# Kernel optimization log

Measured on AMD Instinct MI355X. Metric: run time of the kernel, lower is better.

## Reference

```python
import jax, jax.numpy as jnp
import numpy as np

K = 16  # number of piecewise-linear intervals (fixed in params_set)


def setup_inputs() -> dict:
    key = jax.random.key(0)
    k1, k2 = jax.random.split(key)
    B, S, D = 4, 4096, 2048
    x = jax.random.normal(k1, (B, S, D), dtype=jnp.float32)
    threshold = jnp.ones((1,), dtype=jnp.float32)          # alpha > 0
    theta = 0.1 * jax.random.normal(k2, (K,), dtype=jnp.float32)
    dst = jnp.arange(K, dtype=jnp.float32) / K             # delta * arange(K), delta = 1/K
    return {
        "x": x,
        "threshold": threshold,
        "theta": theta,
        "dst": dst,
        "Qn": 0,
        "Qp": 15,                 # 2**4 - 1 (activation, num_bits=4)
        "num_elements": B * S * D,
    }


def reference(x, threshold, theta, dst, Qn, Qp, num_elements):
    # LCQ_quantizer.forward (non 2-bit-weight path) -> LCQ_fast_core.forward
    s = float(Qp)
    theta_tmp = jax.nn.softmax(theta)                       # softmax over dim 0
    gamma = theta_tmp * K                                   # theta_tmp / delta
    beta = jnp.concatenate(
        [jnp.zeros((1,), theta_tmp.dtype), jnp.cumsum(theta_tmp)[: K - 1]]
    )
    alpha = threshold                                       # shape (1,), broadcasts

    flag_middle = (jnp.abs(x) < alpha).astype(x.dtype)
    flag_high = 1.0 - flag_middle
    x_tmp = jnp.abs(x) / alpha

    # compress: searchsorted bin lookup + piecewise affine
    idx = jnp.searchsorted(dst, x_tmp, side="right")        # in [1, K]
    y = gamma[idx - 1] * (x_tmp - dst[idx - 1]) + beta[idx - 1]
    y_q = jnp.round(y * s) / s                              # uniform round-quantize

    # expand: second searchsorted + inverse affine
    idx_q = jnp.searchsorted(beta, y_q, side="right")       # in [1, K]
    z_mid = (y_q - beta[idx_q - 1]) / gamma[idx_q - 1] + dst[idx_q - 1]

    z = jnp.sign(x) * alpha * (z_mid * flag_middle + flag_high)
    return z
```

## Files before the change

### kernel.cpp

```cpp
#include <hip/hip_runtime.h>
#include <math.h>

#define KB 16

typedef float vf4 __attribute__((ext_vector_type(4)));

__device__ __forceinline__ float lcq_core(float xv, float alpha, float rcp_alpha,
                                          const float2* __restrict__ s_gb,
                                          const float* __restrict__ s_zval)
{
    float a   = fabsf(xv);
    float xt  = __fmul_rn(a, rcp_alpha);
    float t16 = __fmul_rn(xt, 16.0f);
    float jf  = fminf(t16, 15.0f);
    int   j   = (int)jf;
    float2 gb = s_gb[j];
    float dj  = __fmul_rn(floorf(jf), 0.0625f);
    float y   = __fadd_rn(__fmul_rn(gb.x, __fsub_rn(xt, dj)), gb.y);
    float t   = rintf(__fmul_rn(y, 15.0f));
    int   m   = (int)fminf(t, 15.0f);
    float v   = (a < alpha) ? s_zval[m] : 1.0f;
    float r   = __fmul_rn(alpha, v);
    return copysignf(r, xv);
}

__global__ __launch_bounds__(256) void lcq_kernel(
    const float* __restrict__ x,
    const float* __restrict__ thr,
    const float* __restrict__ theta,
    float* __restrict__ out,
    long long n)
{
    __shared__ float2 s_gb[KB];
    __shared__ float  s_zval[KB];
    __shared__ float  s_scal[2];

    if (threadIdx.x == 0) {
        float th[KB];
        float mx = theta[0];
        th[0] = mx;
        #pragma unroll
        for (int i = 1; i < KB; ++i) { th[i] = theta[i]; mx = fmaxf(mx, th[i]); }
        float ex[KB];
        float sum = 0.0f;
        #pragma unroll
        for (int i = 0; i < KB; ++i) { ex[i] = expf(__fsub_rn(th[i], mx)); sum = __fadd_rn(sum, ex[i]); }
        float sm[KB];
        #pragma unroll
        for (int i = 0; i < KB; ++i) sm[i] = __fdiv_rn(ex[i], sum);

        float beta[KB], gamma[KB];
        beta[0] = 0.0f;
        float c = sm[0];
        #pragma unroll
        for (int i = 1; i < KB; ++i) { beta[i] = c; c = __fadd_rn(c, sm[i]); }
        #pragma unroll
        for (int i = 0; i < KB; ++i) gamma[i] = __fmul_rn(sm[i], 16.0f);

        #pragma unroll
        for (int i = 0; i < KB; ++i) s_gb[i] = make_float2(gamma[i], beta[i]);

        for (int m = 0; m < KB; ++m) {
            float yq = __fdiv_rn((float)m, 15.0f);
            int iq = 0;
            #pragma unroll
            for (int i = 1; i < KB; ++i) iq += (beta[i] <= yq) ? 1 : 0;
            s_zval[m] = __fadd_rn(__fdiv_rn(__fsub_rn(yq, beta[iq]), gamma[iq]),
                                  (float)iq * 0.0625f);
        }
        float alpha = thr[0];
        s_scal[0] = alpha;
        s_scal[1] = __fdiv_rn(1.0f, alpha);
    }
    __syncthreads();

    const float alpha = s_scal[0];
    const float rcpa  = s_scal[1];

    const long long tid = (long long)blockIdx.x * blockDim.x + threadIdx.x;
    const long long NT  = (long long)gridDim.x * blockDim.x;
    const long long n4  = n >> 2;

    const vf4* __restrict__ x4 = (const vf4*)x;
    vf4* __restrict__ o4 = (vf4*)out;

    long long i = tid;
    for (; i + 3 * NT < n4; i += 4 * NT) {
        vf4 v0 = __builtin_nontemporal_load(&x4[i]);
        vf4 v1 = __builtin_nontemporal_load(&x4[i + NT]);
        vf4 v2 = __builtin_nontemporal_load(&x4[i + 2 * NT]);
        vf4 v3 = __builtin_nontemporal_load(&x4[i + 3 * NT]);
        vf4 r0, r1, r2, r3;
        r0.x = lcq_core(v0.x, alpha, rcpa, s_gb, s_zval);
        r0.y = lcq_core(v0.y, alpha, rcpa, s_gb, s_zval);
        r0.z = lcq_core(v0.z, alpha, rcpa, s_gb, s_zval);
        r0.w = lcq_core(v0.w, alpha, rcpa, s_gb, s_zval);
        r1.x = lcq_core(v1.x, alpha, rcpa, s_gb, s_zval);
        r1.y = lcq_core(v1.y, alpha, rcpa, s_gb, s_zval);
        r1.z = lcq_core(v1.z, alpha, rcpa, s_gb, s_zval);
        r1.w = lcq_core(v1.w, alpha, rcpa, s_gb, s_zval);
        r2.x = lcq_core(v2.x, alpha, rcpa, s_gb, s_zval);
        r2.y = lcq_core(v2.y, alpha, rcpa, s_gb, s_zval);
        r2.z = lcq_core(v2.z, alpha, rcpa, s_gb, s_zval);
        r2.w = lcq_core(v2.w, alpha, rcpa, s_gb, s_zval);
        r3.x = lcq_core(v3.x, alpha, rcpa, s_gb, s_zval);
        r3.y = lcq_core(v3.y, alpha, rcpa, s_gb, s_zval);
        r3.z = lcq_core(v3.z, alpha, rcpa, s_gb, s_zval);
        r3.w = lcq_core(v3.w, alpha, rcpa, s_gb, s_zval);
        __builtin_nontemporal_store(r0, &o4[i]);
        __builtin_nontemporal_store(r1, &o4[i + NT]);
        __builtin_nontemporal_store(r2, &o4[i + 2 * NT]);
        __builtin_nontemporal_store(r3, &o4[i + 3 * NT]);
    }
    for (; i < n4; i += NT) {
        vf4 v = x4[i];
        vf4 r;
        r.x = lcq_core(v.x, alpha, rcpa, s_gb, s_zval);
        r.y = lcq_core(v.y, alpha, rcpa, s_gb, s_zval);
        r.z = lcq_core(v.z, alpha, rcpa, s_gb, s_zval);
        r.w = lcq_core(v.w, alpha, rcpa, s_gb, s_zval);
        o4[i] = r;
    }
    for (long long k = (n4 << 2) + tid; k < n; k += NT) {
        out[k] = lcq_core(x[k], alpha, rcpa, s_gb, s_zval);
    }
}

extern "C" void kernel_launch(void* const* d_in, const int* in_sizes, int n_in,
                              void* d_out, int out_size, void* d_ws, size_t ws_size,
                              hipStream_t stream) {
    const float* x     = (const float*)d_in[0];
    const float* thr   = (const float*)d_in[1];
    const float* theta = (const float*)d_in[2];
    float* out = (float*)d_out;

    long long n = (long long)in_sizes[0];
    dim3 block(256);
    dim3 grid(2048);
    hipLaunchKernelGGL(lcq_kernel, grid, block, 0, stream, x, thr, theta, out, n);
}
```

Measured before the change: 244.3 us.

## Replace grid-stride loop with one-tile-per-block launch sized to input

```diff
diff --git a/kernel.cpp b/kernel.cpp
--- a/kernel.cpp
+++ b/kernel.cpp
@@ -77,19 +77,17 @@
     const float alpha = s_scal[0];
     const float rcpa  = s_scal[1];
 
-    const long long tid = (long long)blockIdx.x * blockDim.x + threadIdx.x;
-    const long long NT  = (long long)gridDim.x * blockDim.x;
-    const long long n4  = n >> 2;
-
+    const long long n4ll = n >> 2;
     const vf4* __restrict__ x4 = (const vf4*)x;
     vf4* __restrict__ o4 = (vf4*)out;
 
-    long long i = tid;
-    for (; i + 3 * NT < n4; i += 4 * NT) {
-        vf4 v0 = __builtin_nontemporal_load(&x4[i]);
-        vf4 v1 = __builtin_nontemporal_load(&x4[i + NT]);
-        vf4 v2 = __builtin_nontemporal_load(&x4[i + 2 * NT]);
-        vf4 v3 = __builtin_nontemporal_load(&x4[i + 3 * NT]);
+    const unsigned base = blockIdx.x * 1024u + threadIdx.x;
+
+    if ((long long)(blockIdx.x + 1) * 1024ll <= n4ll) {
+        vf4 v0 = __builtin_nontemporal_load(&x4[base]);
+        vf4 v1 = __builtin_nontemporal_load(&x4[base + 256u]);
+        vf4 v2 = __builtin_nontemporal_load(&x4[base + 512u]);
+        vf4 v3 = __builtin_nontemporal_load(&x4[base + 768u]);
         vf4 r0, r1, r2, r3;
         r0.x = lcq_core(v0.x, alpha, rcpa, s_gb, s_zval);
         r0.y = lcq_core(v0.y, alpha, rcpa, s_gb, s_zval);
@@ -107,22 +105,29 @@
         r3.y = lcq_core(v3.y, alpha, rcpa, s_gb, s_zval);
         r3.z = lcq_core(v3.z, alpha, rcpa, s_gb, s_zval);
         r3.w = lcq_core(v3.w, alpha, rcpa, s_gb, s_zval);
-        __builtin_nontemporal_store(r0, &o4[i]);
-        __builtin_nontemporal_store(r1, &o4[i + NT]);
-        __builtin_nontemporal_store(r2, &o4[i + 2 * NT]);
-        __builtin_nontemporal_store(r3, &o4[i + 3 * NT]);
-    }
-    for (; i < n4; i += NT) {
-        vf4 v = x4[i];
-        vf4 r;
-        r.x = lcq_core(v.x, alpha, rcpa, s_gb, s_zval);
-        r.y = lcq_core(v.y, alpha, rcpa, s_gb, s_zval);
-        r.z = lcq_core(v.z, alpha, rcpa, s_gb, s_zval);
-        r.w = lcq_core(v.w, alpha, rcpa, s_gb, s_zval);
-        o4[i] = r;
-    }
-    for (long long k = (n4 << 2) + tid; k < n; k += NT) {
-        out[k] = lcq_core(x[k], alpha, rcpa, s_gb, s_zval);
+        __builtin_nontemporal_store(r0, &o4[base]);
+        __builtin_nontemporal_store(r1, &o4[base + 256u]);
+        __builtin_nontemporal_store(r2, &o4[base + 512u]);
+        __builtin_nontemporal_store(r3, &o4[base + 768u]);
+    } else {
+        #pragma unroll
+        for (int k = 0; k < 4; ++k) {
+            long long i = (long long)base + k * 256;
+            if (i < n4ll) {
+                vf4 v = x4[i];
+                vf4 r;
+                r.x = lcq_core(v.x, alpha, rcpa, s_gb, s_zval);
+                r.y = lcq_core(v.y, alpha, rcpa, s_gb, s_zval);
+                r.z = lcq_core(v.z, alpha, rcpa, s_gb, s_zval);
+                r.w = lcq_core(v.w, alpha, rcpa, s_gb, s_zval);
+                o4[i] = r;
+            }
+        }
+        if (blockIdx.x == gridDim.x - 1) {
+            for (long long k = (n4ll << 2) + threadIdx.x; k < n; k += 256) {
+                out[k] = lcq_core(x[k], alpha, rcpa, s_gb, s_zval);
+            }
+        }
     }
 }
 
@@ -135,7 +140,10 @@
     float* out = (float*)d_out;
 
     long long n = (long long)in_sizes[0];
+    long long n4 = n >> 2;
+    long long grid = (n4 + 1023) / 1024;
+    if (grid < 1) grid = 1;
     dim3 block(256);
-    dim3 grid(2048);
-    hipLaunchKernelGGL(lcq_kernel, grid, block, 0, stream, x, thr, theta, out, n);
+    hipLaunchKernelGGL(lcq_kernel, dim3((unsigned)grid), block, 0, stream,
+                       x, thr, theta, out, n);
 }
```

After: 236.1 us. 1.03x faster.
